# Kernel optimization log

Hardware: AMD Instinct MI355X
Metric: run time of the kernel (lower is better)

## Reference

```python
import jax, jax.numpy as jnp
import numpy as np


def setup_inputs() -> dict:
    key = jax.random.key(0)
    k1, k2, k3, k4 = jax.random.split(key, 4)
    B, N, dim, heads, dim_head = 4, 1025, 768, 12, 64
    inner = heads * dim_head
    x = jax.random.normal(k1, (B, N, dim), dtype=jnp.float32)
    # binary occlusion mask over the N-1 patch tokens (CLS handled inside forward)
    mask = (jax.random.uniform(k2, (B, N - 1, dim)) > 0.5).astype(jnp.float32)
    w_qkv = jax.random.normal(k3, (inner * 3, dim), dtype=jnp.float32) * 0.02
    w_out = jax.random.normal(k4, (dim, inner), dtype=jnp.float32) * 0.02
    b_out = jnp.zeros((dim,), dtype=jnp.float32)
    return {"x": x, "mask": mask, "w_qkv": w_qkv, "w_out": w_out, "b_out": b_out, "heads": heads}


def reference(x, mask, w_qkv, w_out, b_out, heads):
    B, N, dim = x.shape
    inner = w_qkv.shape[0] // 3
    d = inner // heads
    scale = d ** -0.5

    def split_heads(t):  # [B, n, h*d] -> [B, h, n, d]
        return t.reshape(B, t.shape[1], heads, d).transpose(0, 2, 1, 3)

    qkv = x @ w_qkv.T  # [B, N, 3*inner]
    q, k, v = map(split_heads, jnp.split(qkv, 3, axis=-1))

    # --- mask propagation (torch.no_grad block) ---
    mask_sg = jax.lax.stop_gradient(mask)
    qkv_m = mask_sg @ jax.lax.stop_gradient(jnp.abs(w_qkv)).T  # [B, N-1, 3*inner]

    def norm_mask(t):
        t = split_heads(t)  # [B, h, N-1, d]
        t = t / (1e-6 + jnp.max(t, axis=2, keepdims=True))
        return jnp.concatenate([jnp.ones_like(t[:, :, :1]), t], axis=2)  # [B, h, N, d]

    q_m, k_m, v_m = map(norm_mask, jnp.split(qkv_m, 3, axis=-1))
    updated = (jnp.mean(mask_sg, axis=-1, keepdims=True) > 0.0).astype(x.dtype)  # [B, N-1, 1]
    updated = jnp.concatenate([jnp.ones_like(updated[:, :1]), updated], axis=1)  # [B, N, 1]

    # --- masked attention ---
    dots = jnp.einsum('bhnd,bhmd->bhnm', q * q_m, k * k_m) * scale
    attn = jax.nn.softmax(dots, axis=-1)
    out = jnp.einsum('bhnm,bhmd->bhnd', attn, v_m * v)
    out = out.transpose(0, 2, 1, 3).reshape(B, N, inner) * updated
    out = out @ w_out.T + b_out

    # --- mask output propagation (no grad) ---
    m = jax.lax.stop_gradient(jnp.einsum('bhnm,bhmd->bhnd', attn, v_m))
    m = m.transpose(0, 2, 1, 3).reshape(B, N, inner) * updated
    m = m @ jax.lax.stop_gradient(jnp.abs(w_out)).T
    return (out, m[:, 1:])
```

## Files before the change

kernel.cpp:

```cpp
#include <hip/hip_runtime.h>
#include <cmath>

#define TPB 256

static const int NTOK  = 1025;
static const int DIM   = 768;
static const int HEADS = 12;
static const int QK3   = 2304;
static const int ROWS  = 4 * NTOK;
static const int MROWS = 4 * (NTOK - 1);
static const int MPAD  = 4224;
static const int NPAD  = 1088;
static const size_t OUT0 = (size_t)ROWS * DIM;
static const size_t APLANE = (size_t)MPAD * DIM;

static const size_t OFF_QKV16  = 0;
static const size_t OFF_QKVM16 = 4800000;
static const size_t OFF_QE     = 9600000;
static const size_t OFF_KF     = 11300000;
static const size_t OFF_VF     = 13000000;
static const size_t OFF_ABF    = 16400000;
static const size_t OFF_WQ     = 19700000;
static const size_t OFF_WO     = 21500000;
static const size_t OFF_CMAX   = 22100000;
static const size_t OFF_UPD    = 22110000;

typedef __attribute__((ext_vector_type(8))) short short8;
typedef __attribute__((ext_vector_type(4))) float f32x4;

__device__ __forceinline__ unsigned short f2bf(float f) {
    union { float f; unsigned int u; } c; c.f = f;
    unsigned int u = c.u + 0x7fffu + ((c.u >> 16) & 1u);
    return (unsigned short)(u >> 16);
}
__device__ __forceinline__ float bf2f(unsigned short u) {
    union { unsigned int u; float f; } c; c.u = (unsigned int)u << 16;
    return c.f;
}
__device__ __forceinline__ unsigned int cvtpk(float a, float b) {
    unsigned int r;
    asm("v_cvt_pk_bf16_f32 %0, %1, %2" : "=v"(r) : "v"(a), "v"(b));
    return r;
}
__device__ __forceinline__ void gl_lds16(const unsigned short* g, unsigned short* l) {
    __builtin_amdgcn_global_load_lds(
        (const __attribute__((address_space(1))) unsigned int*)g,
        (__attribute__((address_space(3))) unsigned int*)l, 16, 0, 0);
}

__global__ __launch_bounds__(TPB)
void k_cvt(const float* __restrict__ x, const float* __restrict__ mask,
           const float* __restrict__ wqkv, const float* __restrict__ wout,
           unsigned short* __restrict__ Abf, unsigned short* __restrict__ Wq,
           unsigned short* __restrict__ Wo, float* __restrict__ upd,
           float* __restrict__ cmax)
{
    const int z = blockIdx.z;
    if (z == 4) {
        const int bx = blockIdx.x;
        if (bx < 1025) {
            const int w = threadIdx.x >> 6, lane = threadIdx.x & 63;
            const int r = bx * 4 + w;
            if (r >= ROWS) return;
            const int b = r / NTOK, n = r % NTOK;
            float res = 1.f;
            if (n > 0) {
                const float* p = mask + (size_t)(b * (NTOK - 1) + (n - 1)) * DIM;
                float s = 0.f;
                for (int i = lane; i < DIM; i += 64) s += p[i];
#pragma unroll
                for (int off = 32; off > 0; off >>= 1) s += __shfl_xor(s, off, 64);
                res = (s > 0.f) ? 1.f : 0.f;
            }
            if (lane == 0) upd[r] = res;
        } else if (bx < 1034) {
            const int i4 = (bx - 1025) * 256 + threadIdx.x;
            *(float4*)(cmax + (size_t)i4 * 4) = (float4){0.f, 0.f, 0.f, 0.f};
        }
        return;
    }
    const size_t idx = ((size_t)blockIdx.x * TPB + threadIdx.x) * 8;
    unsigned short o[8] __attribute__((aligned(16)));
    if (z <= 1) {
        if (idx >= APLANE) return;
        const int row = (int)(idx / DIM);
        const int M = z ? MROWS : ROWS;
        const float* src = z ? mask : x;
        if (row < M) {
            float a[8];
            *(float4*)&a[0] = *(const float4*)(src + idx);
            *(float4*)&a[4] = *(const float4*)(src + idx + 4);
#pragma unroll
            for (int i = 0; i < 8; ++i) o[i] = f2bf(a[i]);
        } else {
#pragma unroll
            for (int i = 0; i < 8; ++i) o[i] = 0;
        }
        *(short8*)(Abf + (size_t)z * APLANE + idx) = *(short8*)o;
    } else {
        const size_t tot = (z == 2) ? (size_t)QK3 * DIM : (size_t)DIM * DIM;
        if (idx >= tot) return;
        const float* src = (z == 2) ? wqkv : wout;
        unsigned short* dst = (z == 2) ? Wq : Wo;
        float a[8];
        *(float4*)&a[0] = *(const float4*)(src + idx);
        *(float4*)&a[4] = *(const float4*)(src + idx + 4);
        unsigned short oa[8] __attribute__((aligned(16)));
#pragma unroll
        for (int i = 0; i < 8; ++i) { o[i] = f2bf(a[i]); oa[i] = f2bf(fabsf(a[i])); }
        *(short8*)(dst + idx) = *(short8*)o;
        *(short8*)(dst + tot + idx) = *(short8*)oa;
    }
}

__global__ __launch_bounds__(TPB)
void k_gemm_qkv_mfma(const unsigned short* __restrict__ Abf,
                     const unsigned short* __restrict__ Wq,
                     unsigned short* __restrict__ qkv16,
                     unsigned short* __restrict__ qkvm16,
                     float* __restrict__ cmax)
{
    const int bid = blockIdx.x;
    const int xcd = bid & 7, rr = bid >> 3;
    const int id = (xcd < 4) ? (xcd * 149 + rr) : (596 + (xcd - 4) * 148 + rr);
    const int z = id / 594;
    const int rem = id - z * 594;
    const int by = rem / 18, bx = rem - by * 18;
    const int rowT = by * 128, colT = bx * 128;
    if (z == 1 && rowT >= MROWS) return;
    const unsigned short* A = Abf + (size_t)z * APLANE;
    const unsigned short* B = Wq + (size_t)z * QK3 * DIM;

    __shared__ unsigned short As[2][128 * 64];
    __shared__ unsigned short Bs[2][128 * 64];

    const int t = threadIdx.x;
    const int w = t >> 6, lane = t & 63, l15 = lane & 15, quad = lane >> 4;
    const int wm = (w & 1) * 64, wn = (w >> 1) * 64;

    auto stage = [&](int buf, int k0) {
#pragma unroll
        for (int p = 0; p < 4; ++p) {
            const int i = p * 256 + t;
            const int row = i >> 3, ch = i & 7;
            const int gc = k0 + ((ch ^ (row & 7)) << 3);
            gl_lds16(A + (size_t)(rowT + row) * DIM + gc, As[buf] + (size_t)i * 8);
            gl_lds16(B + (size_t)(colT + row) * DIM + gc, Bs[buf] + (size_t)i * 8);
        }
    };

    f32x4 acc[4][4];
#pragma unroll
    for (int i = 0; i < 4; ++i)
#pragma unroll
        for (int j = 0; j < 4; ++j) acc[i][j] = (f32x4){0.f, 0.f, 0.f, 0.f};

    stage(0, 0);
#pragma clang loop unroll(disable)
    for (int kt = 0; kt < 12; ++kt) {
        const int cur = kt & 1;
        if (kt < 11) {
            stage(cur ^ 1, (kt + 1) * 64);
            asm volatile("s_waitcnt vmcnt(8)" ::: "memory");
        } else {
            asm volatile("s_waitcnt vmcnt(0)" ::: "memory");
        }
        __builtin_amdgcn_s_barrier();
        __builtin_amdgcn_sched_barrier(0);
        const unsigned short* as = As[cur];
        const unsigned short* bs = Bs[cur];
        short8 fa[2][4], fb[2][4];
#pragma unroll
        for (int kk = 0; kk < 2; ++kk) {
            const int rc = ((kk * 4 + quad) ^ (l15 & 7)) << 3;
#pragma unroll
            for (int mi = 0; mi < 4; ++mi) {
                fa[kk][mi] = *(const short8*)(as + (wm + mi * 16 + l15) * 64 + rc);
                fb[kk][mi] = *(const short8*)(bs + (wn + mi * 16 + l15) * 64 + rc);
            }
        }
        __builtin_amdgcn_s_setprio(1);
#pragma unroll
        for (int kk = 0; kk < 2; ++kk)
#pragma unroll
            for (int mi = 0; mi < 4; ++mi)
#pragma unroll
                for (int ni = 0; ni < 4; ++ni)
                    acc[mi][ni] = __builtin_amdgcn_mfma_f32_16x16x32_bf16(fa[kk][mi], fb[kk][ni], acc[mi][ni], 0, 0, 0);
        __builtin_amdgcn_s_setprio(0);
        asm volatile("s_waitcnt lgkmcnt(0)" ::: "memory");
        __builtin_amdgcn_s_barrier();
    }

    float cm[4] = {0.f, 0.f, 0.f, 0.f};
#pragma unroll
    for (int mi = 0; mi < 4; ++mi)
#pragma unroll
        for (int ni = 0; ni < 4; ++ni) {
            const int col = colT + wn + ni * 16 + l15;
#pragma unroll
            for (int r = 0; r < 4; ++r) {
                const int row = rowT + wm + mi * 16 + quad * 4 + r;
                const float v = acc[mi][ni][r];
                if (z == 0) {
                    if (row < ROWS) qkv16[(size_t)row * QK3 + col] = f2bf(v);
                } else {
                    qkvm16[(size_t)row * QK3 + col] = f2bf(v);
                    cm[ni] = fmaxf(cm[ni], v);
                }
            }
        }
    if (z == 1) {
        const int bb = rowT >> 10;
#pragma unroll
        for (int ni = 0; ni < 4; ++ni) {
            float m = cm[ni];
            m = fmaxf(m, __shfl_xor(m, 16, 64));
            m = fmaxf(m, __shfl_xor(m, 32, 64));
            if (quad == 0)
                atomicMax((int*)&cmax[bb * QK3 + colT + wn + ni * 16 + l15], __float_as_int(m));
        }
    }
}

__global__ __launch_bounds__(TPB)
void k_prep(const unsigned short* __restrict__ qkv16,
            const unsigned short* __restrict__ qkvm16,
            const float* __restrict__ cmax, unsigned short* __restrict__ qe,
            unsigned short* __restrict__ kfrag, unsigned short* __restrict__ vfrag)
{
    __shared__ unsigned short Vt_l[128 * 66];
    const int t = threadIdx.x;
    const int nt = blockIdx.x, h = blockIdx.y, b = blockIdx.z;
    const int bh = b * HEADS + h;
    const int nl = t >> 2, ds0 = (t & 3) * 16;
    const int n = nt * 64 + nl;
    const bool valid = n < NTOK;
    const int col0 = h * 64 + ds0;

    unsigned short q16[16] __attribute__((aligned(16))) = {0};
    unsigned short k16[16] __attribute__((aligned(16))) = {0};
    unsigned short v16[16] __attribute__((aligned(16))) = {0};
    unsigned short qm16[16] __attribute__((aligned(16)));
    unsigned short km16[16] __attribute__((aligned(16)));
    unsigned short vm16[16] __attribute__((aligned(16)));
    float cq[16], ck[16], cv[16];

    const bool useM = valid && (n > 0);
    if (valid) {
        const size_t br = (size_t)(b * NTOK + n) * QK3 + col0;
        *(short8*)&q16[0] = *(const short8*)(qkv16 + br);
        *(short8*)&q16[8] = *(const short8*)(qkv16 + br + 8);
        *(short8*)&k16[0] = *(const short8*)(qkv16 + br + 768);
        *(short8*)&k16[8] = *(const short8*)(qkv16 + br + 776);
        *(short8*)&v16[0] = *(const short8*)(qkv16 + br + 1536);
        *(short8*)&v16[8] = *(const short8*)(qkv16 + br + 1544);
    }
    if (useM) {
        const size_t mr = (size_t)(b * 1024 + (n - 1)) * QK3 + col0;
        *(short8*)&qm16[0] = *(const short8*)(qkvm16 + mr);
        *(short8*)&qm16[8] = *(const short8*)(qkvm16 + mr + 8);
        *(short8*)&km16[0] = *(const short8*)(qkvm16 + mr + 768);
        *(short8*)&km16[8] = *(const short8*)(qkvm16 + mr + 776);
        *(short8*)&vm16[0] = *(const short8*)(qkvm16 + mr + 1536);
        *(short8*)&vm16[8] = *(const short8*)(qkvm16 + mr + 1544);
        const int cb = b * QK3 + col0;
#pragma unroll
        for (int i = 0; i < 4; ++i) {
            *(float4*)&cq[i * 4] = *(const float4*)(cmax + cb + i * 4);
            *(float4*)&ck[i * 4] = *(const float4*)(cmax + cb + 768 + i * 4);
            *(float4*)&cv[i * 4] = *(const float4*)(cmax + cb + 1536 + i * 4);
        }
    }

    unsigned short oq[16] __attribute__((aligned(16)));
    unsigned short ok[16] __attribute__((aligned(16)));
#pragma unroll
    for (int idx = 0; idx < 16; ++idx) {
        const float qm = useM ? bf2f(qm16[idx]) / (1e-6f + cq[idx]) : 1.f;
        const float km = useM ? bf2f(km16[idx]) / (1e-6f + ck[idx]) : 1.f;
        const float vm = valid ? (useM ? bf2f(vm16[idx]) / (1e-6f + cv[idx]) : 1.f) : 0.f;
        oq[idx] = f2bf(bf2f(q16[idx]) * qm * 0.18033688f);
        ok[idx] = f2bf(bf2f(k16[idx]) * km);
        const int d = ds0 + idx;
        Vt_l[d * 66 + nl]        = f2bf(bf2f(v16[idx]) * vm);
        Vt_l[(64 + d) * 66 + nl] = f2bf(vm);
    }
    {
        unsigned short* qp = qe + ((size_t)bh * NPAD + n) * 64 + ds0;
        *(short8*)qp       = *(short8*)oq;
        *(short8*)(qp + 8) = *(short8*)(oq + 8);
    }
    {
        const int nc = nl >> 4, l15 = nl & 15;
        const int kk = ds0 >> 5, qb = (ds0 & 31) >> 3;
        unsigned short* kp = kfrag + (((size_t)bh * 17 + nt) * 8 + kk * 4 + nc) * 512;
        *(short8*)(kp + ((size_t)(qb * 16 + l15)) * 8)       = *(short8*)ok;
        *(short8*)(kp + ((size_t)((qb + 1) * 16 + l15)) * 8) = *(short8*)(ok + 8);
    }
    __syncthreads();
    const int c = t >> 1, nh = (t & 1) * 32;
    unsigned short ov[32] __attribute__((aligned(16)));
#pragma unroll
    for (int i = 0; i < 32; ++i) ov[i] = Vt_l[c * 66 + nh + i];
    const int c8 = c >> 4, l15v = c & 15, kkv = nh >> 5;
    unsigned short* vp = vfrag + (((size_t)bh * 17 + nt) * 16 + c8 * 2 + kkv) * 512 + (size_t)l15v * 8;
#pragma unroll
    for (int qd = 0; qd < 4; ++qd)
        *(short8*)(vp + (size_t)qd * 128) = *(short8*)(ov + qd * 8);
}

__global__ __launch_bounds__(64, 2)
void k_attn(const unsigned short* __restrict__ qe, const unsigned short* __restrict__ kfrag,
            const unsigned short* __restrict__ vfrag, const float* __restrict__ upd,
            unsigned short* __restrict__ ab2)
{
    const int flat = blockIdx.y * 33 + blockIdx.x;
    const int d2 = (flat & 7) * 198 + (flat >> 3);
    const int bh = d2 / 33, qt = d2 - bh * 33;
    const int b = bh / HEADS, h = bh - b * HEADS;
    const int lane = threadIdx.x;
    const int l15 = lane & 15, quad = lane >> 4;
    const int q0 = qt * 32;

    short8 qf[2][2];
#pragma unroll
    for (int j = 0; j < 2; ++j) {
        const unsigned short* qp = qe + ((size_t)bh * NPAD + q0 + j * 16 + l15) * 64 + (quad << 3);
        qf[j][0] = *(const short8*)qp;
        qf[j][1] = *(const short8*)(qp + 32);
    }
    const int pA = (quad & 1) * 32 + l15;
    const int pB = pA + 16;
    const bool lo32 = (lane < 32);

    const unsigned short* kb = kfrag + (size_t)bh * (17 * 8 * 512) + (size_t)lane * 8;
    const unsigned short* vb = vfrag + (size_t)bh * (17 * 16 * 512) + (size_t)lane * 8;

    short8 kf[8], vf[16];
#pragma unroll
    for (int g = 0; g < 8; ++g) kf[g] = *(const short8*)(kb + g * 512);
#pragma unroll
    for (int g = 0; g < 16; ++g) vf[g] = *(const short8*)(vb + g * 512);

    f32x4 acc[2][8];
    float lac[2] = {0.f, 0.f};
#pragma unroll
    for (int j = 0; j < 2; ++j)
#pragma unroll
        for (int g = 0; g < 8; ++g) acc[j][g] = (f32x4){0.f, 0.f, 0.f, 0.f};

    const float EC = 14.4269504f;

#pragma clang loop unroll(disable)
    for (int kt = 0; kt < 17; ++kt) {
        f32x4 s[2][4];
        __builtin_amdgcn_s_setprio(1);
#pragma unroll
        for (int nc = 0; nc < 4; ++nc) {
#pragma unroll
            for (int j = 0; j < 2; ++j) {
                f32x4 z = (f32x4){0.f, 0.f, 0.f, 0.f};
                z = __builtin_amdgcn_mfma_f32_16x16x32_bf16(kf[nc], qf[j][0], z, 0, 0, 0);
                z = __builtin_amdgcn_mfma_f32_16x16x32_bf16(kf[4 + nc], qf[j][1], z, 0, 0, 0);
                s[j][nc] = z;
            }
        }
        __builtin_amdgcn_s_setprio(0);
        if (kt < 16) {
            const unsigned short* kn = kb + (size_t)(kt + 1) * 4096;
#pragma unroll
            for (int g = 0; g < 8; ++g) kf[g] = *(const short8*)(kn + g * 512);
        }
        short8 pf[2][2];
#pragma unroll
        for (int j = 0; j < 2; ++j) {
            unsigned int dA[4], dB[4];
            float psum = 0.f, p00 = 0.f;
#pragma unroll
            for (int nc = 0; nc < 4; ++nc) {
                const float p0 = __builtin_amdgcn_exp2f(s[j][nc][0] - EC);
                const float p1 = __builtin_amdgcn_exp2f(s[j][nc][1] - EC);
                const float p2 = __builtin_amdgcn_exp2f(s[j][nc][2] - EC);
                const float p3 = __builtin_amdgcn_exp2f(s[j][nc][3] - EC);
                dA[nc] = cvtpk(p0, p1);
                dB[nc] = cvtpk(p2, p3);
                psum += (p0 + p1) + (p2 + p3);
                if (nc == 0) p00 = p0;
            }
            if (kt < 16) lac[j] += psum;
            else if (quad == 0) lac[j] += p00;
            union { int i[4]; short8 s; } u0, u1;
            {
                const int a0 = __shfl((int)dA[0], pA, 64), a1 = __shfl((int)dA[1], pA, 64);
                const int b0 = __shfl((int)dB[0], pA, 64), b1 = __shfl((int)dB[1], pA, 64);
                const int a2 = __shfl((int)dA[0], pB, 64), a3 = __shfl((int)dA[1], pB, 64);
                const int b2 = __shfl((int)dB[0], pB, 64), b3 = __shfl((int)dB[1], pB, 64);
                u0.i[0] = lo32 ? a0 : a1;
                u0.i[1] = lo32 ? b0 : b1;
                u0.i[2] = lo32 ? a2 : a3;
                u0.i[3] = lo32 ? b2 : b3;
            }
            {
                const int a0 = __shfl((int)dA[2], pA, 64), a1 = __shfl((int)dA[3], pA, 64);
                const int b0 = __shfl((int)dB[2], pA, 64), b1 = __shfl((int)dB[3], pA, 64);
                const int a2 = __shfl((int)dA[2], pB, 64), a3 = __shfl((int)dA[3], pB, 64);
                const int b2 = __shfl((int)dB[2], pB, 64), b3 = __shfl((int)dB[3], pB, 64);
                u1.i[0] = lo32 ? a0 : a1;
                u1.i[1] = lo32 ? b0 : b1;
                u1.i[2] = lo32 ? a2 : a3;
                u1.i[3] = lo32 ? b2 : b3;
            }
            pf[j][0] = u0.s;
            pf[j][1] = u1.s;
        }
        __builtin_amdgcn_s_setprio(1);
#pragma unroll
        for (int g = 0; g < 8; ++g) {
#pragma unroll
            for (int j = 0; j < 2; ++j) {
                acc[j][g] = __builtin_amdgcn_mfma_f32_16x16x32_bf16(vf[2 * g],     pf[j][0], acc[j][g], 0, 0, 0);
                acc[j][g] = __builtin_amdgcn_mfma_f32_16x16x32_bf16(vf[2 * g + 1], pf[j][1], acc[j][g], 0, 0, 0);
            }
        }
        __builtin_amdgcn_s_setprio(0);
        if (kt < 16) {
            const unsigned short* vn = vb + (size_t)(kt + 1) * 8192;
#pragma unroll
            for (int g = 0; g < 16; ++g) vf[g] = *(const short8*)(vn + g * 512);
        }
    }

#pragma unroll
    for (int j = 0; j < 2; ++j) {
        float lq = lac[j];
        lq += __shfl_xor(lq, 16, 64);
        lq += __shfl_xor(lq, 32, 64);
        const int qrow = q0 + j * 16 + l15;
        if (qrow < NTOK) {
            const size_t rg = (size_t)b * NTOK + qrow;
            const float inv = upd[rg] / lq;
#pragma unroll
            for (int g = 0; g < 8; ++g) {
                uint2 pk;
                pk.x = cvtpk(acc[j][g][0] * inv, acc[j][g][1] * inv);
                pk.y = cvtpk(acc[j][g][2] * inv, acc[j][g][3] * inv);
                const size_t addr = (size_t)(g >> 2) * APLANE + rg * DIM + h * 64 + (g & 3) * 16 + quad * 4;
                *(uint2*)(ab2 + addr) = pk;
            }
        }
    }
}

__global__ __launch_bounds__(TPB)
void k_gemm_out_mfma(const unsigned short* __restrict__ ab2,
                     const unsigned short* __restrict__ Wo,
                     const float* __restrict__ bout, float* __restrict__ dout)
{
    const int bid = blockIdx.x;
    const int xcd = bid & 7, rr = bid >> 3;
    const int id = (xcd < 4) ? (xcd * 50 + rr) : (200 + (xcd - 4) * 49 + rr);
    const int z = id / 198;
    const int rem = id - z * 198;
    const int by = rem / 6, bx = rem - by * 6;
    const int rowT = by * 128, colT = bx * 128;

    const unsigned short* A = ab2 + (size_t)z * APLANE;
    const unsigned short* B = Wo + (size_t)z * DIM * DIM;

    __shared__ unsigned short As[2][128 * 64];
    __shared__ unsigned short Bs[2][128 * 64];

    const int t = threadIdx.x;
    const int w = t >> 6, lane = t & 63, l15 = lane & 15, quad = lane >> 4;
    const int wm = (w & 1) * 64, wn = (w >> 1) * 64;

    auto stage = [&](int buf, int k0) {
#pragma unroll
        for (int p = 0; p < 4; ++p) {
            const int i = p * 256 + t;
            const int row = i >> 3, ch = i & 7;
            const int gc = k0 + ((ch ^ (row & 7)) << 3);
            gl_lds16(A + (size_t)(rowT + row) * DIM + gc, As[buf] + (size_t)i * 8);
            gl_lds16(B + (size_t)(colT + row) * DIM + gc, Bs[buf] + (size_t)i * 8);
        }
    };

    f32x4 acc[4][4];
#pragma unroll
    for (int i = 0; i < 4; ++i)
#pragma unroll
        for (int j = 0; j < 4; ++j) acc[i][j] = (f32x4){0.f, 0.f, 0.f, 0.f};

    stage(0, 0);
#pragma clang loop unroll(disable)
    for (int kt = 0; kt < 12; ++kt) {
        const int cur = kt & 1;
        if (kt < 11) {
            stage(cur ^ 1, (kt + 1) * 64);
            asm volatile("s_waitcnt vmcnt(8)" ::: "memory");
        } else {
            asm volatile("s_waitcnt vmcnt(0)" ::: "memory");
        }
        __builtin_amdgcn_s_barrier();
        __builtin_amdgcn_sched_barrier(0);
        const unsigned short* as = As[cur];
        const unsigned short* bs = Bs[cur];
        short8 fa[2][4], fb[2][4];
#pragma unroll
        for (int kk = 0; kk < 2; ++kk) {
            const int rc = ((kk * 4 + quad) ^ (l15 & 7)) << 3;
#pragma unroll
            for (int mi = 0; mi < 4; ++mi) {
                fa[kk][mi] = *(const short8*)(as + (wm + mi * 16 + l15) * 64 + rc);
                fb[kk][mi] = *(const short8*)(bs + (wn + mi * 16 + l15) * 64 + rc);
            }
        }
        __builtin_amdgcn_s_setprio(1);
#pragma unroll
        for (int kk = 0; kk < 2; ++kk)
#pragma unroll
            for (int mi = 0; mi < 4; ++mi)
#pragma unroll
                for (int ni = 0; ni < 4; ++ni)
                    acc[mi][ni] = __builtin_amdgcn_mfma_f32_16x16x32_bf16(fa[kk][mi], fb[kk][ni], acc[mi][ni], 0, 0, 0);
        __builtin_amdgcn_s_setprio(0);
        asm volatile("s_waitcnt lgkmcnt(0)" ::: "memory");
        __builtin_amdgcn_s_barrier();
    }

#pragma unroll
    for (int mi = 0; mi < 4; ++mi)
#pragma unroll
        for (int ni = 0; ni < 4; ++ni) {
            const int col = colT + wn + ni * 16 + l15;
            const float bb = (z == 0) ? bout[col] : 0.f;
#pragma unroll
            for (int r = 0; r < 4; ++r) {
                const int row = rowT + wm + mi * 16 + quad * 4 + r;
                if (row >= ROWS) continue;
                const int b = row / NTOK, n = row % NTOK;
                if (z == 0) {
                    dout[(size_t)row * DIM + col] = acc[mi][ni][r] + bb;
                } else if (n >= 1) {
                    dout[OUT0 + ((size_t)(b * (NTOK - 1) + (n - 1))) * DIM + col] = acc[mi][ni][r];
                }
            }
        }
}

extern "C" void kernel_launch(void* const* d_in, const int* in_sizes, int n_in,
                              void* d_out, int out_size, void* d_ws, size_t ws_size,
                              hipStream_t stream)
{
    const float* x    = (const float*)d_in[0];
    const float* mask = (const float*)d_in[1];
    const float* wqkv = (const float*)d_in[2];
    const float* wout = (const float*)d_in[3];
    const float* bout = (const float*)d_in[4];
    float* ws = (float*)d_ws;
    unsigned short* qkv16  = (unsigned short*)(ws + OFF_QKV16);
    unsigned short* qkvm16 = (unsigned short*)(ws + OFF_QKVM16);
    unsigned short* qe  = (unsigned short*)(ws + OFF_QE);
    unsigned short* kfr = (unsigned short*)(ws + OFF_KF);
    unsigned short* vfr = (unsigned short*)(ws + OFF_VF);
    unsigned short* abf = (unsigned short*)(ws + OFF_ABF);
    unsigned short* wq  = (unsigned short*)(ws + OFF_WQ);
    unsigned short* wo  = (unsigned short*)(ws + OFF_WO);
    float* cmax = ws + OFF_CMAX;
    float* upd  = ws + OFF_UPD;
    float* out  = (float*)d_out;

    hipLaunchKernelGGL(k_cvt,           dim3(1584, 1, 5), dim3(TPB), 0, stream, x, mask, wqkv, wout, abf, wq, wo, upd, cmax);
    hipLaunchKernelGGL(k_gemm_qkv_mfma, dim3(1188),       dim3(TPB), 0, stream, abf, wq, qkv16, qkvm16, cmax);
    hipLaunchKernelGGL(k_prep,          dim3(17, 12, 4),  dim3(TPB), 0, stream, qkv16, qkvm16, cmax, qe, kfr, vfr);
    hipLaunchKernelGGL(k_attn,          dim3(33, 48),     dim3(64),  0, stream, qe, kfr, vfr, upd, abf);
    hipLaunchKernelGGL(k_gemm_out_mfma, dim3(396),        dim3(TPB), 0, stream, abf, wo, bout, out);
}
```

Before: 214.8 us.

## Use 256x128 QKV GEMM tiles with split staging and fuse mask-row test into conversion

The QKV GEMM moves to 512-thread blocks with 256x128 tiles, which halves the block count and raises reuse of B-operand loads. The prefetch of the next k-slice is split into two halves interleaved with the two MFMA sub-steps. The per-row mask-nonzero test now runs inside the bf16 conversion pass, using a memset plus per-chunk writes in place of a separate wave reduction that reread the mask. The larger tile raises LDS and register pressure. The fused test checks whether any 8-element chunk has a positive sum, which matches the reference's row-mean test only because mask values are non-negative.

Result: no change. 214.0 us (-0.3%).

```diff
diff --git a/kernel.cpp b/kernel.cpp
--- a/kernel.cpp
+++ b/kernel.cpp
@@ -58,23 +58,10 @@
     const int z = blockIdx.z;
     if (z == 4) {
         const int bx = blockIdx.x;
-        if (bx < 1025) {
-            const int w = threadIdx.x >> 6, lane = threadIdx.x & 63;
-            const int r = bx * 4 + w;
-            if (r >= ROWS) return;
-            const int b = r / NTOK, n = r % NTOK;
-            float res = 1.f;
-            if (n > 0) {
-                const float* p = mask + (size_t)(b * (NTOK - 1) + (n - 1)) * DIM;
-                float s = 0.f;
-                for (int i = lane; i < DIM; i += 64) s += p[i];
-#pragma unroll
-                for (int off = 32; off > 0; off >>= 1) s += __shfl_xor(s, off, 64);
-                res = (s > 0.f) ? 1.f : 0.f;
-            }
-            if (lane == 0) upd[r] = res;
-        } else if (bx < 1034) {
-            const int i4 = (bx - 1025) * 256 + threadIdx.x;
+        if (bx == 0) {
+            if (threadIdx.x < 4) upd[threadIdx.x * NTOK] = 1.f;
+        } else if (bx < 10) {
+            const int i4 = (bx - 1) * 256 + threadIdx.x;
             *(float4*)(cmax + (size_t)i4 * 4) = (float4){0.f, 0.f, 0.f, 0.f};
         }
         return;
@@ -92,6 +79,13 @@
             *(float4*)&a[4] = *(const float4*)(src + idx + 4);
 #pragma unroll
             for (int i = 0; i < 8; ++i) o[i] = f2bf(a[i]);
+            if (z == 1) {
+                const float s = ((a[0] + a[1]) + (a[2] + a[3])) + ((a[4] + a[5]) + (a[6] + a[7]));
+                if (s > 0.f) {
+                    const int b = row >> 10, j = row & 1023;
+                    upd[b * NTOK + j + 1] = 1.f;
+                }
+            }
         } else {
 #pragma unroll
             for (int i = 0; i < 8; ++i) o[i] = 0;
@@ -113,7 +107,7 @@
     }
 }
 
-__global__ __launch_bounds__(TPB)
+__global__ __launch_bounds__(512)
 void k_gemm_qkv_mfma(const unsigned short* __restrict__ Abf,
                      const unsigned short* __restrict__ Wq,
                      unsigned short* __restrict__ qkv16,
@@ -122,30 +116,34 @@
 {
     const int bid = blockIdx.x;
     const int xcd = bid & 7, rr = bid >> 3;
-    const int id = (xcd < 4) ? (xcd * 149 + rr) : (596 + (xcd - 4) * 148 + rr);
-    const int z = id / 594;
-    const int rem = id - z * 594;
-    const int by = rem / 18, bx = rem - by * 18;
-    const int rowT = by * 128, colT = bx * 128;
-    if (z == 1 && rowT >= MROWS) return;
+    const int id = (xcd < 2) ? (xcd * 75 + rr) : (150 + (xcd - 2) * 74 + rr);
+    int z, by, bx;
+    if (id < 306) { z = 0; by = id / 18; bx = id - by * 18; }
+    else          { const int r2 = id - 306; z = 1; by = r2 / 18; bx = r2 - by * 18; }
+    const int rowT = by * 256, colT = bx * 128;
     const unsigned short* A = Abf + (size_t)z * APLANE;
     const unsigned short* B = Wq + (size_t)z * QK3 * DIM;
 
-    __shared__ unsigned short As[2][128 * 64];
+    __shared__ unsigned short As[2][256 * 64];
     __shared__ unsigned short Bs[2][128 * 64];
 
     const int t = threadIdx.x;
     const int w = t >> 6, lane = t & 63, l15 = lane & 15, quad = lane >> 4;
-    const int wm = (w & 1) * 64, wn = (w >> 1) * 64;
-
-    auto stage = [&](int buf, int k0) {
-#pragma unroll
-        for (int p = 0; p < 4; ++p) {
-            const int i = p * 256 + t;
-            const int row = i >> 3, ch = i & 7;
+    const int wm = (w & 3) * 64, wn = (w >> 2) * 64;
+
+    auto stageH = [&](int buf, int k0, int h) {
+#pragma unroll
+        for (int p = 0; p < 2; ++p) {
+            const int i2 = (h * 2 + p) * 512 + t;
+            const int row = i2 >> 3, ch = i2 & 7;
             const int gc = k0 + ((ch ^ (row & 7)) << 3);
-            gl_lds16(A + (size_t)(rowT + row) * DIM + gc, As[buf] + (size_t)i * 8);
-            gl_lds16(B + (size_t)(colT + row) * DIM + gc, Bs[buf] + (size_t)i * 8);
+            gl_lds16(A + (size_t)(rowT + row) * DIM + gc, As[buf] + (size_t)i2 * 8);
+        }
+        {
+            const int i2 = h * 512 + t;
+            const int row = i2 >> 3, ch = i2 & 7;
+            const int gc = k0 + ((ch ^ (row & 7)) << 3);
+            gl_lds16(B + (size_t)(colT + row) * DIM + gc, Bs[buf] + (size_t)i2 * 8);
         }
     };
 
@@ -155,13 +153,14 @@
 #pragma unroll
         for (int j = 0; j < 4; ++j) acc[i][j] = (f32x4){0.f, 0.f, 0.f, 0.f};
 
-    stage(0, 0);
+    stageH(0, 0, 0); stageH(0, 0, 1);
+
 #pragma clang loop unroll(disable)
     for (int kt = 0; kt < 12; ++kt) {
         const int cur = kt & 1;
         if (kt < 11) {
-            stage(cur ^ 1, (kt + 1) * 64);
-            asm volatile("s_waitcnt vmcnt(8)" ::: "memory");
+            stageH(cur ^ 1, (kt + 1) * 64, 0);
+            asm volatile("s_waitcnt vmcnt(3)" ::: "memory");
         } else {
             asm volatile("s_waitcnt vmcnt(0)" ::: "memory");
         }
@@ -169,24 +168,38 @@
         __builtin_amdgcn_sched_barrier(0);
         const unsigned short* as = As[cur];
         const unsigned short* bs = Bs[cur];
-        short8 fa[2][4], fb[2][4];
-#pragma unroll
-        for (int kk = 0; kk < 2; ++kk) {
-            const int rc = ((kk * 4 + quad) ^ (l15 & 7)) << 3;
+        short8 fa[4], fb[4];
+        {
+            const int rc = (quad ^ (l15 & 7)) << 3;
 #pragma unroll
             for (int mi = 0; mi < 4; ++mi) {
-                fa[kk][mi] = *(const short8*)(as + (wm + mi * 16 + l15) * 64 + rc);
-                fb[kk][mi] = *(const short8*)(bs + (wn + mi * 16 + l15) * 64 + rc);
+                fa[mi] = *(const short8*)(as + (wm + mi * 16 + l15) * 64 + rc);
+                fb[mi] = *(const short8*)(bs + (wn + mi * 16 + l15) * 64 + rc);
             }
         }
         __builtin_amdgcn_s_setprio(1);
 #pragma unroll
-        for (int kk = 0; kk < 2; ++kk)
-#pragma unroll
-            for (int mi = 0; mi < 4; ++mi)
-#pragma unroll
-                for (int ni = 0; ni < 4; ++ni)
-                    acc[mi][ni] = __builtin_amdgcn_mfma_f32_16x16x32_bf16(fa[kk][mi], fb[kk][ni], acc[mi][ni], 0, 0, 0);
+        for (int mi = 0; mi < 4; ++mi)
+#pragma unroll
+            for (int ni = 0; ni < 4; ++ni)
+                acc[mi][ni] = __builtin_amdgcn_mfma_f32_16x16x32_bf16(fa[mi], fb[ni], acc[mi][ni], 0, 0, 0);
+        __builtin_amdgcn_s_setprio(0);
+        short8 ga[4], gb[4];
+        {
+            const int rc = ((4 + quad) ^ (l15 & 7)) << 3;
+#pragma unroll
+            for (int mi = 0; mi < 4; ++mi) {
+                ga[mi] = *(const short8*)(as + (wm + mi * 16 + l15) * 64 + rc);
+                gb[mi] = *(const short8*)(bs + (wn + mi * 16 + l15) * 64 + rc);
+            }
+        }
+        if (kt < 11) stageH(cur ^ 1, (kt + 1) * 64, 1);
+        __builtin_amdgcn_s_setprio(1);
+#pragma unroll
+        for (int mi = 0; mi < 4; ++mi)
+#pragma unroll
+            for (int ni = 0; ni < 4; ++ni)
+                acc[mi][ni] = __builtin_amdgcn_mfma_f32_16x16x32_bf16(ga[mi], gb[ni], acc[mi][ni], 0, 0, 0);
         __builtin_amdgcn_s_setprio(0);
         asm volatile("s_waitcnt lgkmcnt(0)" ::: "memory");
         __builtin_amdgcn_s_barrier();
@@ -571,8 +584,9 @@
     float* upd  = ws + OFF_UPD;
     float* out  = (float*)d_out;
 
+    hipMemsetAsync(upd, 0, ROWS * sizeof(float), stream);
     hipLaunchKernelGGL(k_cvt,           dim3(1584, 1, 5), dim3(TPB), 0, stream, x, mask, wqkv, wout, abf, wq, wo, upd, cmax);
-    hipLaunchKernelGGL(k_gemm_qkv_mfma, dim3(1188),       dim3(TPB), 0, stream, abf, wq, qkv16, qkvm16, cmax);
+    hipLaunchKernelGGL(k_gemm_qkv_mfma, dim3(594),        dim3(512), 0, stream, abf, wq, qkv16, qkvm16, cmax);
     hipLaunchKernelGGL(k_prep,          dim3(17, 12, 4),  dim3(TPB), 0, stream, qkv16, qkvm16, cmax, qe, kfr, vfr);
     hipLaunchKernelGGL(k_attn,          dim3(33, 48),     dim3(64),  0, stream, qe, kfr, vfr, upd, abf);
     hipLaunchKernelGGL(k_gemm_out_mfma, dim3(396),        dim3(TPB), 0, stream, abf, wo, bout, out);
```
